# Optimization experiments

Measured on AMD Instinct MI355X. Metric: run time of the kernel, lower is better.

## Reference

```python
import jax, jax.numpy as jnp
import numpy as np

EMB = 512
NUM_HEAD = 8
HEAD_DIM = EMB // NUM_HEAD  # 64
B, S = 16, 2048


def setup_inputs() -> dict:
    key = jax.random.key(0)
    k1, k2, k3, k4 = jax.random.split(key, 4)
    x1 = jax.random.normal(k1, (B, S, EMB), dtype=jnp.float32)
    # causal mask: 1 where attention allowed, 0 elsewhere (masked_fill where mask==0)
    mask = jnp.tril(jnp.ones((S, S), dtype=jnp.int32))
    scale = 1.0 / np.sqrt(EMB)
    Wq = jax.random.normal(k2, (EMB, HEAD_DIM), dtype=jnp.float32) * scale
    Wk = jax.random.normal(k3, (EMB, HEAD_DIM), dtype=jnp.float32) * scale
    Wv = jax.random.normal(k4, (EMB, HEAD_DIM), dtype=jnp.float32) * scale
    return {"x1": x1, "mask": mask, "Wq": Wq, "Wk": Wk, "Wv": Wv}


def reference(x1, mask, Wq, Wk, Wv):
    # q,k,v: [B,S,H]
    q = jnp.einsum('bse,eh->bsh', x1, Wq)
    k = jnp.einsum('bse,eh->bsh', x1, Wk)
    v = jnp.einsum('bse,eh->bsh', x1, Wv)
    # scores: [B,S,S]
    scaled_qk = jnp.einsum('bqh,bkh->bqk', q, k) / jnp.sqrt(jnp.float32(HEAD_DIM))
    scaled_qk = jnp.where(mask == 0, -jnp.inf, scaled_qk)
    attn = jax.nn.softmax(scaled_qk, axis=-1)
    return jnp.einsum('bqk,bkh->bqh', attn, v)
```

## Files before the change

kernel.cpp:

```cpp
#include <hip/hip_runtime.h>
#include <hip/hip_bf16.h>

typedef __attribute__((ext_vector_type(8))) short bf16x8;
typedef __attribute__((ext_vector_type(4))) float f32x4;
typedef __attribute__((ext_vector_type(4))) unsigned short u16x4;

#define MFMA16(a, b, c) __builtin_amdgcn_mfma_f32_16x16x32_bf16(a, b, c, 0, 0, 0)

#define QSCALE 0.18033688011112042f

#define GLDS16(gp, lp)                                                         \
    __builtin_amdgcn_global_load_lds(                                          \
        (const __attribute__((address_space(1))) void*)(gp),                   \
        (__attribute__((address_space(3))) void*)(lp), 16, 0, 0)

__device__ __forceinline__ short nbf(float f) {
    __hip_bfloat16 h = __float2bfloat16(f);
    return *(short*)&h;
}
__device__ __forceinline__ unsigned short nbfu(float f) {
    __hip_bfloat16 h = __float2bfloat16(f);
    return *(unsigned short*)&h;
}

__global__ void wt_kernel(const float* __restrict__ Wq, const float* __restrict__ Wk,
                          const float* __restrict__ Wv, unsigned short* __restrict__ Wt) {
    const int h = blockIdx.x;
    const int mat = blockIdx.y;
    const int e = threadIdx.x;
    const float* W = (mat == 0) ? Wq : ((mat == 1) ? Wk : Wv);
    Wt[(mat * 64 + h) * 512 + e] = nbfu(W[e * 64 + h]);
}

__global__ __launch_bounds__(512, 1) void qkv_proj(
    const float* __restrict__ x1, const unsigned short* __restrict__ Wt,
    unsigned short* __restrict__ Q, unsigned short* __restrict__ Kf,
    unsigned short* __restrict__ Vf)
{
    __shared__ char alds[2][16384];
    __shared__ char blds[2][12288];

    const int tid = threadIdx.x;
    const int W = tid >> 6, lane = tid & 63;
    const int c = lane & 15, g = lane >> 4;
    const int tokB = blockIdx.x * 128;

    const char* x1b = (const char*)x1;
    const char* Wtb = (const char*)Wt;

    const int tA0 = tid >> 3,           qA0 = (tid & 7) ^ (tA0 & 7);
    const int tA1 = (tid + 512) >> 3,   qA1 = (tid & 7) ^ (tA1 & 7);
    const size_t aoff0 = (size_t)(tokB + tA0) * 2048 + qA0 * 16;
    const size_t aoff1 = (size_t)(tokB + tA1) * 2048 + qA1 * 16;

    auto bsrc = [&](int j) -> size_t {
        const int n = j >> 6, c2 = (j >> 2) & 15, g2 = j & 3;
        return (size_t)((n >> 2) * 64 + (n & 3) * 16 + c2) * 1024 + g2 * 16;
    };
    const size_t boff0 = bsrc(tid), boff1 = bsrc(tid + 512);

    f32x4 acc[12];
#pragma unroll
    for (int n = 0; n < 12; ++n) acc[n] = (f32x4)0.f;

    GLDS16(x1b + aoff0, &alds[0][tid * 16]);
    GLDS16(x1b + aoff1, &alds[0][8192 + tid * 16]);
    GLDS16(Wtb + boff0, &blds[0][tid * 16]);
    if (tid < 256) GLDS16(Wtb + boff1, &blds[0][8192 + tid * 16]);

    const int arow = (W * 16 + c) * 128;
    const int aq0 = (((2 * g) ^ (c & 7)) * 16);
    const int aq1 = (((2 * g + 1) ^ (c & 7)) * 16);
    const int brd = (c * 4 + g) * 16;

    int buf = 0;
    for (int ks = 0; ks < 16; ++ks) {
        asm volatile("s_waitcnt vmcnt(0)\n\ts_barrier" ::: "memory");

        if (ks < 15) {
            const size_t ka = (size_t)(ks + 1) * 128;
            const size_t kb = (size_t)(ks + 1) * 64;
            char* ab = &alds[buf ^ 1][0];
            char* bb = &blds[buf ^ 1][0];
            GLDS16(x1b + aoff0 + ka, ab + tid * 16);
            GLDS16(x1b + aoff1 + ka, ab + 8192 + tid * 16);
            GLDS16(Wtb + boff0 + kb, bb + tid * 16);
            if (tid < 256) GLDS16(Wtb + boff1 + kb, bb + 8192 + tid * 16);
        }

        const char* ab = &alds[buf][0];
        const char* bb = &blds[buf][0];
        f32x4 a0 = *(const f32x4*)(ab + arow + aq0);
        f32x4 a1 = *(const f32x4*)(ab + arow + aq1);
        bf16x8 af;
        af[0] = nbf(a0[0]); af[1] = nbf(a0[1]); af[2] = nbf(a0[2]); af[3] = nbf(a0[3]);
        af[4] = nbf(a1[0]); af[5] = nbf(a1[1]); af[6] = nbf(a1[2]); af[7] = nbf(a1[3]);
#pragma unroll
        for (int n = 0; n < 12; ++n) {
            bf16x8 bf = *(const bf16x8*)(bb + n * 1024 + brd);
            acc[n] = MFMA16(af, bf, acc[n]);
        }
        buf ^= 1;
    }

    const int tok0 = tokB + W * 16;
    const int bb2 = tokB >> 11;
    const int ht = ((tokB & 2047) >> 6) + (W >> 2);

#pragma unroll
    for (int n = 0; n < 4; ++n)
#pragma unroll
        for (int r = 0; r < 4; ++r)
            Q[(size_t)(tok0 + g * 4 + r) * 64 + n * 16 + c] = nbfu(acc[n][r] * QSCALE);

    {
        unsigned short* kf = Kf + (size_t)bb2 * 131072 + (size_t)ht * 4096;
#pragma unroll
        for (int n = 0; n < 4; ++n) {
            const int gf = (n & 1) * 2 + (c >> 3);
            const size_t base = (size_t)(n >> 1) * 2048 + (W & 3) * 512 + (c & 7);
#pragma unroll
            for (int r = 0; r < 4; ++r)
                kf[base + (size_t)(gf * 16 + g * 4 + r) * 8] = nbfu(acc[4 + n][r]);
        }
    }

    {
        unsigned short* vf = Vf + (size_t)bb2 * 131072 + (size_t)ht * 4096;
        const int sub = (W & 3) >> 1;
        const int gf = (W & 1) * 2 + (g >> 1);
        const int jb = (g & 1) * 4;
#pragma unroll
        for (int n = 0; n < 4; ++n) {
            u16x4 pv;
#pragma unroll
            for (int r = 0; r < 4; ++r) pv[r] = nbfu(acc[8 + n][r]);
            *(u16x4*)(vf + (size_t)sub * 2048 + n * 512 + (gf * 16 + c) * 8 + jb) = pv;
        }
    }
}

__global__ __launch_bounds__(512, 4) void flash_attn(
    const unsigned short* __restrict__ Q, const unsigned short* __restrict__ Kf,
    const unsigned short* __restrict__ Vf, float* __restrict__ out)
{
    __shared__ char p_lds[32768];
    __shared__ float mb[4][16], lb[4][16];

    const int tid = threadIdx.x;
    const int W = tid >> 6;
    const int st = W >> 2;
    const int w = W & 3;
    const int lane = tid & 63;
    const int c = lane & 15, g = lane >> 4;

    const int id = blockIdx.x;
    const int b = 2 * (id & 7) + ((id >> 3) & 1);
    const int k = id >> 4;
    const int qt = (k < 16) ? (31 - k) : (k - 16);
    const int n2 = (qt >> 1) + 1;
    const int qr0c = qt * 64 + w * 16 + c;
    const size_t qrow_g = ((size_t)b << 11) + qt * 64 + w * 16;

    bf16x8 qf0 = *(const bf16x8*)(Q + (qrow_g + c) * 64 + g * 8);
    bf16x8 qf1 = *(const bf16x8*)(Q + (qrow_g + c) * 64 + 32 + g * 8);

    const char* Kfb = (const char*)(Kf + (size_t)b * 131072);
    const char* Vfb = (const char*)(Vf + (size_t)b * 131072);

    float m = -1e30f, l = 0.f;
    f32x4 acc[4];
#pragma unroll
    for (int n = 0; n < 4; ++n) acc[n] = (f32x4)0.f;

    for (int t = st; t < n2; t += 2) {
        const char* kt = Kfb + (size_t)t * 16384;
        const char* vt = Vfb + (size_t)t * 16384;

        f32x4 s[8];
#pragma unroll
        for (int i = 0; i < 8; ++i) s[i] = (f32x4)0.f;
#pragma unroll
        for (int h = 0; h < 2; ++h) {
            bf16x8 ka[4], kb2[4];
#pragma unroll
            for (int n = 0; n < 4; ++n) {
                ka[n]  = *(const bf16x8*)(kt + h * 8192 + n * 1024 + lane * 16);
                kb2[n] = *(const bf16x8*)(kt + h * 8192 + 4096 + n * 1024 + lane * 16);
            }
            __builtin_amdgcn_s_setprio(1);
#pragma unroll
            for (int n = 0; n < 4; ++n) {
                s[h * 4 + n] = MFMA16(ka[n], qf0, s[h * 4 + n]);
                s[h * 4 + n] = MFMA16(kb2[n], qf1, s[h * 4 + n]);
            }
            __builtin_amdgcn_s_setprio(0);
        }

        if (t == n2 - 1) {
#pragma unroll
            for (int h = 0; h < 2; ++h)
#pragma unroll
                for (int n = 0; n < 4; ++n) {
                    const int key0 = t * 128 + h * 64 + n * 16 + g * 4;
#pragma unroll
                    for (int r = 0; r < 4; ++r)
                        if (key0 + r > qr0c) s[h * 4 + n][r] = -1e30f;
                }
        }

        float tm = -1e30f;
#pragma unroll
        for (int i = 0; i < 8; ++i)
            tm = fmaxf(tm, fmaxf(fmaxf(s[i][0], s[i][1]), fmaxf(s[i][2], s[i][3])));

        if (__any(tm > m + 8.f)) {
            float gm = tm;
            gm = fmaxf(gm, __shfl_xor(gm, 16, 64));
            gm = fmaxf(gm, __shfl_xor(gm, 32, 64));
            const float mn = fmaxf(m, gm);
            const float alpha = exp2f(m - mn);
            m = mn;
            l *= alpha;
            float al[4];
#pragma unroll
            for (int r = 0; r < 4; ++r) al[r] = __shfl(alpha, g * 4 + r, 16);
#pragma unroll
            for (int n = 0; n < 4; ++n)
#pragma unroll
                for (int r = 0; r < 4; ++r) acc[n][r] *= al[r];
        }

        char* pw = &p_lds[W * 4096 + ((g >> 1) * 16 + c) * 16 + (g & 1) * 8];
#pragma unroll
        for (int h = 0; h < 2; ++h)
#pragma unroll
            for (int n = 0; n < 4; ++n) {
                const int i = h * 4 + n;
                float p0 = exp2f(s[i][0] - m);
                float p1 = exp2f(s[i][1] - m);
                float p2 = exp2f(s[i][2] - m);
                float p3 = exp2f(s[i][3] - m);
                l += (p0 + p1) + (p2 + p3);
                u16x4 pk;
                pk[0] = nbfu(p0); pk[1] = nbfu(p1); pk[2] = nbfu(p2); pk[3] = nbfu(p3);
                *(u16x4*)(pw + (h * 2 + (n >> 1)) * 1024 + (n & 1) * 512) = pk;
            }

        const char* pr = &p_lds[W * 4096 + lane * 16];
#pragma unroll
        for (int ps = 0; ps < 4; ++ps) {
            bf16x8 pf = *(const bf16x8*)(pr + ps * 1024);
            bf16x8 vf[4];
#pragma unroll
            for (int n = 0; n < 4; ++n)
                vf[n] = *(const bf16x8*)(vt + (ps >> 1) * 8192 + (ps & 1) * 4096 + n * 1024 + lane * 16);
            __builtin_amdgcn_s_setprio(1);
#pragma unroll
            for (int n = 0; n < 4; ++n)
                acc[n] = MFMA16(pf, vf[n], acc[n]);
            __builtin_amdgcn_s_setprio(0);
        }
    }

    __syncthreads();
    float* accb = (float*)&p_lds[0];

    if (st == 1) {
        l += __shfl_xor(l, 16, 64);
        l += __shfl_xor(l, 32, 64);
        if (g == 0) { mb[w][c] = m; lb[w][c] = l; }
#pragma unroll
        for (int n = 0; n < 4; ++n)
#pragma unroll
            for (int r = 0; r < 4; ++r)
                accb[w * 1024 + (g * 4 + r) * 64 + n * 16 + c] = acc[n][r];
    }
    __syncthreads();

    if (st == 0) {
        l += __shfl_xor(l, 16, 64);
        l += __shfl_xor(l, 32, 64);
        const float m1c = mb[w][c];
        const float l1c = lb[w][c];
        const float mF = fmaxf(m, m1c);
        const float a0 = exp2f(m - mF);
        const float a1 = (m1c > -1e29f) ? exp2f(m1c - mF) : 0.f;
        const float inv = 1.f / (l * a0 + l1c * a1);
        const float s0 = a0 * inv, s1 = a1 * inv;
        float s0r[4], s1r[4];
#pragma unroll
        for (int r = 0; r < 4; ++r) {
            s0r[r] = __shfl(s0, g * 4 + r, 16);
            s1r[r] = __shfl(s1, g * 4 + r, 16);
        }
#pragma unroll
        for (int n = 0; n < 4; ++n)
#pragma unroll
            for (int r = 0; r < 4; ++r) {
                const float a1v = accb[w * 1024 + (g * 4 + r) * 64 + n * 16 + c];
                out[(qrow_g + g * 4 + r) * 64 + n * 16 + c] = acc[n][r] * s0r[r] + a1v * s1r[r];
            }
    }
}

extern "C" void kernel_launch(void* const* d_in, const int* in_sizes, int n_in,
                              void* d_out, int out_size, void* d_ws, size_t ws_size,
                              hipStream_t stream) {
    const float* x1 = (const float*)d_in[0];
    const float* Wq = (const float*)d_in[2];
    const float* Wk = (const float*)d_in[3];
    const float* Wv = (const float*)d_in[4];
    float* out = (float*)d_out;

    unsigned short* Wt  = (unsigned short*)d_ws;
    unsigned short* Qw  = (unsigned short*)((char*)d_ws + 196608);
    unsigned short* Kfw = (unsigned short*)((char*)d_ws + 196608 + 4194304);
    unsigned short* Vfw = (unsigned short*)((char*)d_ws + 196608 + 2 * 4194304);

    wt_kernel<<<dim3(64, 3), 512, 0, stream>>>(Wq, Wk, Wv, Wt);
    qkv_proj<<<256, 512, 0, stream>>>(x1, Wt, Qw, Kfw, Vfw);
    flash_attn<<<512, 512, 0, stream>>>(Qw, Kfw, Vfw, out);
}
```

Baseline: 55.79 us.

## Give each wave two query sub-tiles and split keys four ways

```diff
diff --git a/kernel.cpp b/kernel.cpp
--- a/kernel.cpp
+++ b/kernel.cpp
@@ -140,17 +140,17 @@
     }
 }
 
-__global__ __launch_bounds__(512, 4) void flash_attn(
+__global__ __launch_bounds__(512, 2) void flash_attn(
     const unsigned short* __restrict__ Q, const unsigned short* __restrict__ Kf,
     const unsigned short* __restrict__ Vf, float* __restrict__ out)
 {
-    __shared__ char p_lds[32768];
-    __shared__ float mb[4][16], lb[4][16];
+    __shared__ char p_lds[65536];
+    __shared__ float mlb[2][2][3][32];
 
     const int tid = threadIdx.x;
     const int W = tid >> 6;
-    const int st = W >> 2;
-    const int w = W & 3;
+    const int st = W & 3;
+    const int qg = W >> 2;
     const int lane = tid & 63;
     const int c = lane & 15, g = lane >> 4;
 
@@ -159,27 +159,31 @@
     const int k = id >> 4;
     const int qt = (k < 16) ? (31 - k) : (k - 16);
     const int n2 = (qt >> 1) + 1;
-    const int qr0c = qt * 64 + w * 16 + c;
-    const size_t qrow_g = ((size_t)b << 11) + qt * 64 + w * 16;
-
-    bf16x8 qf0 = *(const bf16x8*)(Q + (qrow_g + c) * 64 + g * 8);
-    bf16x8 qf1 = *(const bf16x8*)(Q + (qrow_g + c) * 64 + 32 + g * 8);
+    const int qrA = qt * 64 + qg * 32 + c;
+    const int qrB = qrA + 16;
+    const size_t qbase = ((size_t)b << 11) + qt * 64 + qg * 32;
+
+    bf16x8 qfA0 = *(const bf16x8*)(Q + (qbase + c) * 64 + g * 8);
+    bf16x8 qfA1 = *(const bf16x8*)(Q + (qbase + c) * 64 + 32 + g * 8);
+    bf16x8 qfB0 = *(const bf16x8*)(Q + (qbase + 16 + c) * 64 + g * 8);
+    bf16x8 qfB1 = *(const bf16x8*)(Q + (qbase + 16 + c) * 64 + 32 + g * 8);
 
     const char* Kfb = (const char*)(Kf + (size_t)b * 131072);
     const char* Vfb = (const char*)(Vf + (size_t)b * 131072);
 
-    float m = -1e30f, l = 0.f;
-    f32x4 acc[4];
-#pragma unroll
-    for (int n = 0; n < 4; ++n) acc[n] = (f32x4)0.f;
-
-    for (int t = st; t < n2; t += 2) {
+    float mA = -1e30f, lA = 0.f;
+    float mB = -1e30f, lB = 0.f;
+    f32x4 accA[4], accB[4];
+#pragma unroll
+    for (int n = 0; n < 4; ++n) { accA[n] = (f32x4)0.f; accB[n] = (f32x4)0.f; }
+
+    for (int t = st; t < n2; t += 4) {
         const char* kt = Kfb + (size_t)t * 16384;
         const char* vt = Vfb + (size_t)t * 16384;
 
-        f32x4 s[8];
-#pragma unroll
-        for (int i = 0; i < 8; ++i) s[i] = (f32x4)0.f;
+        f32x4 sA[8], sB[8];
+#pragma unroll
+        for (int i = 0; i < 8; ++i) { sA[i] = (f32x4)0.f; sB[i] = (f32x4)0.f; }
 #pragma unroll
         for (int h = 0; h < 2; ++h) {
             bf16x8 ka[4], kb2[4];
@@ -191,8 +195,10 @@
             __builtin_amdgcn_s_setprio(1);
 #pragma unroll
             for (int n = 0; n < 4; ++n) {
-                s[h * 4 + n] = MFMA16(ka[n], qf0, s[h * 4 + n]);
-                s[h * 4 + n] = MFMA16(kb2[n], qf1, s[h * 4 + n]);
+                sA[h * 4 + n] = MFMA16(ka[n], qfA0, sA[h * 4 + n]);
+                sA[h * 4 + n] = MFMA16(kb2[n], qfA1, sA[h * 4 + n]);
+                sB[h * 4 + n] = MFMA16(ka[n], qfB0, sB[h * 4 + n]);
+                sB[h * 4 + n] = MFMA16(kb2[n], qfB1, sB[h * 4 + n]);
             }
             __builtin_amdgcn_s_setprio(0);
         }
@@ -204,103 +210,192 @@
                 for (int n = 0; n < 4; ++n) {
                     const int key0 = t * 128 + h * 64 + n * 16 + g * 4;
 #pragma unroll
-                    for (int r = 0; r < 4; ++r)
-                        if (key0 + r > qr0c) s[h * 4 + n][r] = -1e30f;
+                    for (int r = 0; r < 4; ++r) {
+                        if (key0 + r > qrA) sA[h * 4 + n][r] = -1e30f;
+                        if (key0 + r > qrB) sB[h * 4 + n][r] = -1e30f;
+                    }
                 }
         }
 
-        float tm = -1e30f;
-#pragma unroll
-        for (int i = 0; i < 8; ++i)
-            tm = fmaxf(tm, fmaxf(fmaxf(s[i][0], s[i][1]), fmaxf(s[i][2], s[i][3])));
-
-        if (__any(tm > m + 8.f)) {
-            float gm = tm;
-            gm = fmaxf(gm, __shfl_xor(gm, 16, 64));
-            gm = fmaxf(gm, __shfl_xor(gm, 32, 64));
-            const float mn = fmaxf(m, gm);
-            const float alpha = exp2f(m - mn);
-            m = mn;
-            l *= alpha;
-            float al[4];
-#pragma unroll
-            for (int r = 0; r < 4; ++r) al[r] = __shfl(alpha, g * 4 + r, 16);
-#pragma unroll
-            for (int n = 0; n < 4; ++n)
-#pragma unroll
-                for (int r = 0; r < 4; ++r) acc[n][r] *= al[r];
-        }
-
-        char* pw = &p_lds[W * 4096 + ((g >> 1) * 16 + c) * 16 + (g & 1) * 8];
-#pragma unroll
-        for (int h = 0; h < 2; ++h)
-#pragma unroll
-            for (int n = 0; n < 4; ++n) {
-                const int i = h * 4 + n;
-                float p0 = exp2f(s[i][0] - m);
-                float p1 = exp2f(s[i][1] - m);
-                float p2 = exp2f(s[i][2] - m);
-                float p3 = exp2f(s[i][3] - m);
-                l += (p0 + p1) + (p2 + p3);
-                u16x4 pk;
-                pk[0] = nbfu(p0); pk[1] = nbfu(p1); pk[2] = nbfu(p2); pk[3] = nbfu(p3);
-                *(u16x4*)(pw + (h * 2 + (n >> 1)) * 1024 + (n & 1) * 512) = pk;
-            }
-
-        const char* pr = &p_lds[W * 4096 + lane * 16];
+        {
+            float tm = -1e30f;
+#pragma unroll
+            for (int i = 0; i < 8; ++i)
+                tm = fmaxf(tm, fmaxf(fmaxf(sA[i][0], sA[i][1]), fmaxf(sA[i][2], sA[i][3])));
+            if (__any(tm > mA + 8.f)) {
+                float gm = tm;
+                gm = fmaxf(gm, __shfl_xor(gm, 16, 64));
+                gm = fmaxf(gm, __shfl_xor(gm, 32, 64));
+                const float mn = fmaxf(mA, gm);
+                const float alpha = exp2f(mA - mn);
+                mA = mn;
+                lA *= alpha;
+                float al[4];
+#pragma unroll
+                for (int r = 0; r < 4; ++r) al[r] = __shfl(alpha, g * 4 + r, 16);
+#pragma unroll
+                for (int n = 0; n < 4; ++n)
+#pragma unroll
+                    for (int r = 0; r < 4; ++r) accA[n][r] *= al[r];
+            }
+            char* pw = &p_lds[W * 8192 + ((g >> 1) * 16 + c) * 16 + (g & 1) * 8];
+#pragma unroll
+            for (int h = 0; h < 2; ++h)
+#pragma unroll
+                for (int n = 0; n < 4; ++n) {
+                    const int i = h * 4 + n;
+                    float p0 = exp2f(sA[i][0] - mA);
+                    float p1 = exp2f(sA[i][1] - mA);
+                    float p2 = exp2f(sA[i][2] - mA);
+                    float p3 = exp2f(sA[i][3] - mA);
+                    lA += (p0 + p1) + (p2 + p3);
+                    u16x4 pk;
+                    pk[0] = nbfu(p0); pk[1] = nbfu(p1); pk[2] = nbfu(p2); pk[3] = nbfu(p3);
+                    *(u16x4*)(pw + (h * 2 + (n >> 1)) * 1024 + (n & 1) * 512) = pk;
+                }
+        }
+        {
+            float tm = -1e30f;
+#pragma unroll
+            for (int i = 0; i < 8; ++i)
+                tm = fmaxf(tm, fmaxf(fmaxf(sB[i][0], sB[i][1]), fmaxf(sB[i][2], sB[i][3])));
+            if (__any(tm > mB + 8.f)) {
+                float gm = tm;
+                gm = fmaxf(gm, __shfl_xor(gm, 16, 64));
+                gm = fmaxf(gm, __shfl_xor(gm, 32, 64));
+                const float mn = fmaxf(mB, gm);
+                const float alpha = exp2f(mB - mn);
+                mB = mn;
+                lB *= alpha;
+                float al[4];
+#pragma unroll
+                for (int r = 0; r < 4; ++r) al[r] = __shfl(alpha, g * 4 + r, 16);
+#pragma unroll
+                for (int n = 0; n < 4; ++n)
+#pragma unroll
+                    for (int r = 0; r < 4; ++r) accB[n][r] *= al[r];
+            }
+            char* pw = &p_lds[W * 8192 + 4096 + ((g >> 1) * 16 + c) * 16 + (g & 1) * 8];
+#pragma unroll
+            for (int h = 0; h < 2; ++h)
+#pragma unroll
+                for (int n = 0; n < 4; ++n) {
+                    const int i = h * 4 + n;
+                    float p0 = exp2f(sB[i][0] - mB);
+                    float p1 = exp2f(sB[i][1] - mB);
+                    float p2 = exp2f(sB[i][2] - mB);
+                    float p3 = exp2f(sB[i][3] - mB);
+                    lB += (p0 + p1) + (p2 + p3);
+                    u16x4 pk;
+                    pk[0] = nbfu(p0); pk[1] = nbfu(p1); pk[2] = nbfu(p2); pk[3] = nbfu(p3);
+                    *(u16x4*)(pw + (h * 2 + (n >> 1)) * 1024 + (n & 1) * 512) = pk;
+                }
+        }
+
+        const char* prA = &p_lds[W * 8192 + lane * 16];
+        const char* prB = prA + 4096;
 #pragma unroll
         for (int ps = 0; ps < 4; ++ps) {
-            bf16x8 pf = *(const bf16x8*)(pr + ps * 1024);
+            bf16x8 pfA = *(const bf16x8*)(prA + ps * 1024);
+            bf16x8 pfB = *(const bf16x8*)(prB + ps * 1024);
             bf16x8 vf[4];
 #pragma unroll
             for (int n = 0; n < 4; ++n)
                 vf[n] = *(const bf16x8*)(vt + (ps >> 1) * 8192 + (ps & 1) * 4096 + n * 1024 + lane * 16);
             __builtin_amdgcn_s_setprio(1);
 #pragma unroll
-            for (int n = 0; n < 4; ++n)
-                acc[n] = MFMA16(pf, vf[n], acc[n]);
+            for (int n = 0; n < 4; ++n) {
+                accA[n] = MFMA16(pfA, vf[n], accA[n]);
+                accB[n] = MFMA16(pfB, vf[n], accB[n]);
+            }
             __builtin_amdgcn_s_setprio(0);
         }
     }
 
+    lA += __shfl_xor(lA, 16, 64); lA += __shfl_xor(lA, 32, 64);
+    lB += __shfl_xor(lB, 16, 64); lB += __shfl_xor(lB, 32, 64);
     __syncthreads();
     float* accb = (float*)&p_lds[0];
 
-    if (st == 1) {
-        l += __shfl_xor(l, 16, 64);
-        l += __shfl_xor(l, 32, 64);
-        if (g == 0) { mb[w][c] = m; lb[w][c] = l; }
+    if (st != 0) {
+        const int slot = (st - 1) * 2 + qg;
+        if (g == 0) {
+            mlb[0][qg][st - 1][c] = mA;      mlb[0][qg][st - 1][16 + c] = mB;
+            mlb[1][qg][st - 1][c] = lA;      mlb[1][qg][st - 1][16 + c] = lB;
+        }
 #pragma unroll
         for (int n = 0; n < 4; ++n)
 #pragma unroll
-            for (int r = 0; r < 4; ++r)
-                accb[w * 1024 + (g * 4 + r) * 64 + n * 16 + c] = acc[n][r];
+            for (int r = 0; r < 4; ++r) {
+                accb[slot * 2048 + (g * 4 + r) * 64 + n * 16 + c] = accA[n][r];
+                accb[slot * 2048 + (16 + g * 4 + r) * 64 + n * 16 + c] = accB[n][r];
+            }
     }
     __syncthreads();
 
     if (st == 0) {
-        l += __shfl_xor(l, 16, 64);
-        l += __shfl_xor(l, 32, 64);
-        const float m1c = mb[w][c];
-        const float l1c = lb[w][c];
-        const float mF = fmaxf(m, m1c);
-        const float a0 = exp2f(m - mF);
-        const float a1 = (m1c > -1e29f) ? exp2f(m1c - mF) : 0.f;
-        const float inv = 1.f / (l * a0 + l1c * a1);
-        const float s0 = a0 * inv, s1 = a1 * inv;
-        float s0r[4], s1r[4];
-#pragma unroll
-        for (int r = 0; r < 4; ++r) {
-            s0r[r] = __shfl(s0, g * 4 + r, 16);
-            s1r[r] = __shfl(s1, g * 4 + r, 16);
-        }
-#pragma unroll
-        for (int n = 0; n < 4; ++n)
+        {
+            const float m1 = mlb[0][qg][0][c], l1 = mlb[1][qg][0][c];
+            const float m2 = mlb[0][qg][1][c], l2 = mlb[1][qg][1][c];
+            const float m3 = mlb[0][qg][2][c], l3 = mlb[1][qg][2][c];
+            const float mF = fmaxf(fmaxf(mA, m1), fmaxf(m2, m3));
+            const float a0 = exp2f(mA - mF);
+            const float a1 = (m1 > -1e29f) ? exp2f(m1 - mF) : 0.f;
+            const float a2 = (m2 > -1e29f) ? exp2f(m2 - mF) : 0.f;
+            const float a3 = (m3 > -1e29f) ? exp2f(m3 - mF) : 0.f;
+            const float inv = 1.f / (lA * a0 + l1 * a1 + l2 * a2 + l3 * a3);
+            const float s0 = a0 * inv, s1 = a1 * inv, s2 = a2 * inv, s3 = a3 * inv;
+            float s0r[4], s1r[4], s2r[4], s3r[4];
 #pragma unroll
             for (int r = 0; r < 4; ++r) {
-                const float a1v = accb[w * 1024 + (g * 4 + r) * 64 + n * 16 + c];
-                out[(qrow_g + g * 4 + r) * 64 + n * 16 + c] = acc[n][r] * s0r[r] + a1v * s1r[r];
-            }
+                s0r[r] = __shfl(s0, g * 4 + r, 16);
+                s1r[r] = __shfl(s1, g * 4 + r, 16);
+                s2r[r] = __shfl(s2, g * 4 + r, 16);
+                s3r[r] = __shfl(s3, g * 4 + r, 16);
+            }
+#pragma unroll
+            for (int n = 0; n < 4; ++n)
+#pragma unroll
+                for (int r = 0; r < 4; ++r) {
+                    const int ro = (g * 4 + r) * 64 + n * 16 + c;
+                    const float v = accA[n][r] * s0r[r]
+                                  + accb[(0 * 2 + qg) * 2048 + ro] * s1r[r]
+                                  + accb[(1 * 2 + qg) * 2048 + ro] * s2r[r]
+                                  + accb[(2 * 2 + qg) * 2048 + ro] * s3r[r];
+                    out[(qbase + g * 4 + r) * 64 + n * 16 + c] = v;
+                }
+        }
+        {
+            const float m1 = mlb[0][qg][0][16 + c], l1 = mlb[1][qg][0][16 + c];
+            const float m2 = mlb[0][qg][1][16 + c], l2 = mlb[1][qg][1][16 + c];
+            const float m3 = mlb[0][qg][2][16 + c], l3 = mlb[1][qg][2][16 + c];
+            const float mF = fmaxf(fmaxf(mB, m1), fmaxf(m2, m3));
+            const float a0 = exp2f(mB - mF);
+            const float a1 = (m1 > -1e29f) ? exp2f(m1 - mF) : 0.f;
+            const float a2 = (m2 > -1e29f) ? exp2f(m2 - mF) : 0.f;
+            const float a3 = (m3 > -1e29f) ? exp2f(m3 - mF) : 0.f;
+            const float inv = 1.f / (lB * a0 + l1 * a1 + l2 * a2 + l3 * a3);
+            const float s0 = a0 * inv, s1 = a1 * inv, s2 = a2 * inv, s3 = a3 * inv;
+            float s0r[4], s1r[4], s2r[4], s3r[4];
+#pragma unroll
+            for (int r = 0; r < 4; ++r) {
+                s0r[r] = __shfl(s0, g * 4 + r, 16);
+                s1r[r] = __shfl(s1, g * 4 + r, 16);
+                s2r[r] = __shfl(s2, g * 4 + r, 16);
+                s3r[r] = __shfl(s3, g * 4 + r, 16);
+            }
+#pragma unroll
+            for (int n = 0; n < 4; ++n)
+#pragma unroll
+                for (int r = 0; r < 4; ++r) {
+                    const int ro = (16 + g * 4 + r) * 64 + n * 16 + c;
+                    const float v = accB[n][r] * s0r[r]
+                                  + accb[(0 * 2 + qg) * 2048 + ro] * s1r[r]
+                                  + accb[(1 * 2 + qg) * 2048 + ro] * s2r[r]
+                                  + accb[(2 * 2 + qg) * 2048 + ro] * s3r[r];
+                    out[(qbase + 16 + g * 4 + r) * 64 + n * 16 + c] = v;
+                }
+        }
     }
 }
 
```

Result: slower. 61.77 us (+10.7%).
